# Performance work log

Hardware: AMD Instinct MI355X
Metric: run time of the kernel (lower is better)

## Reference

```python
import jax, jax.numpy as jnp
import numpy as np

SCALING = 128.0 / 64  # alpha / rank = 2.0
EPS = 1e-8


def setup_inputs() -> dict:
    key = jax.random.key(0)
    ks = jax.random.split(key, 5)
    B, S, D_IN, D_OUT, R = 2, 4096, 4096, 4096, 64
    x = jax.random.normal(ks[0], (B, S, D_IN), dtype=jnp.float32)
    base_output = jax.random.normal(ks[1], (B, S, D_OUT), dtype=jnp.float32)
    base_weight = jax.random.normal(ks[2], (D_OUT, D_IN), dtype=jnp.float32) * 0.02
    lora_A = jax.random.normal(ks[3], (R, D_IN), dtype=jnp.float32) * 0.02
    lora_B = jax.random.normal(ks[4], (D_OUT, R), dtype=jnp.float32) * 0.02
    magnitude = jnp.ones((D_OUT,), dtype=jnp.float32)
    return {"x": x, "base_output": base_output, "base_weight": base_weight,
            "lora_A": lora_A, "lora_B": lora_B, "magnitude": magnitude}


def reference(x, base_output, base_weight, lora_A, lora_B, magnitude):
    # LoRA path: x @ A^T @ B^T, scaled  (dropout p=0 -> identity)
    xa = jnp.einsum('bsd,rd->bsr', x, lora_A)          # [B,S,r]
    delta_v = jnp.einsum('bsr,or->bso', xa, lora_B) * SCALING  # [B,S,out]
    # Updated weight and its per-row L2 norm
    updated_weight = base_weight + (lora_B @ lora_A) * SCALING  # [out,in]
    updated_norm = jnp.sqrt(jnp.sum(updated_weight * updated_weight, axis=1))  # [out]
    mag_scale = magnitude / (updated_norm + EPS)  # [out]
    combined = base_output + delta_v
    return combined * mag_scale[None, None, :]
```

## Files before the change

### kernel.cpp

```cpp
#include <hip/hip_runtime.h>
#include <math.h>

typedef __bf16 bf16x8 __attribute__((ext_vector_type(8)));
typedef float f32x4 __attribute__((ext_vector_type(4)));

#define MFMA16(a, b, c) __builtin_amdgcn_mfma_f32_16x16x32_bf16(a, b, c, 0, 0, 0)

static constexpr int M_TOT = 8192;
static constexpr int DIN = 4096;
static constexpr int DOUT = 4096;
static constexpr int RNK = 64;

__device__ inline unsigned short f2bf(float f) {
    union { float f; unsigned u; } v; v.f = f;
    unsigned r = v.u + 0x7FFFu + ((v.u >> 16) & 1u);
    return (unsigned short)(r >> 16);
}

__device__ inline void gload_lds16(const float* g, char* lds_base) {
    __builtin_amdgcn_global_load_lds(
        (const __attribute__((address_space(1))) void*)g,
        (__attribute__((address_space(3))) void*)lds_base, 16, 0, 0);
}

__global__ __launch_bounds__(256) void k_prep(const float* __restrict__ A,
                                              const float* __restrict__ B,
                                              unsigned short* __restrict__ Afrag,
                                              unsigned short* __restrict__ Atfrag,
                                              unsigned short* __restrict__ Bfrag) {
    int i = blockIdx.x * 256 + threadIdx.x;
    unsigned short ab = f2bf(A[i]);
    int n = i >> 12, k = i & 4095;
    Afrag[(((k >> 5) << 2) + (n >> 4)) * 512 +
          ((((k >> 3) & 3) << 4) + (n & 15)) * 8 + (k & 7)] = ab;
    Atfrag[(((k >> 4) << 1) + (n >> 5)) * 512 +
           ((((n >> 3) & 3) << 4) + (k & 15)) * 8 + (n & 7)] = ab;
    unsigned short bb = f2bf(B[i]);
    int o = i >> 6, r = i & 63;
    Bfrag[(((o >> 4) << 1) + (r >> 5)) * 512 +
          ((((r >> 3) & 3) << 4) + (o & 15)) * 8 + (r & 7)] = bb;
}

__global__ __launch_bounds__(256) void k1_xa(const float* __restrict__ x,
                                             const unsigned short* __restrict__ Afrag,
                                             float* __restrict__ pxa) {
    __shared__ __align__(16) char smem[32768];
    char* buf0 = smem;
    char* buf1 = smem + 16384;
    float (*red)[1024] = (float (*)[1024])smem;
    int tid = threadIdx.x;
    int wid = tid >> 6, lane = tid & 63;
    int row = lane & 15, kq = lane >> 4;
    int lane8 = lane * 8;
    int mt = blockIdx.x & 511, kpart = blockIdx.x >> 9;
    int m0 = mt * 16;
    int swzr = (row & 7) << 4;
    const float* xbase = x + (size_t)m0 * DIN + kpart * 2048;

    f32x4 acc0 = {0.f, 0.f, 0.f, 0.f};
    f32x4 acc1 = acc0, acc2 = acc0, acc3 = acc0;
    bf16x8 setA[8], setB[8];

    auto STAGE = [&](char* buf, int c) {
        #pragma unroll
        for (int j = 0; j < 4; ++j) {
            int r = wid * 4 + j;
            int srcb = (lane * 16) ^ ((r & 7) << 4);
            const float* g = xbase + (size_t)r * DIN + c * 256 + (srcb >> 2);
            gload_lds16(g, buf + r * 1024);
        }
    };
    auto AFRAG = [&](bf16x8* set, int c) {
        #pragma unroll
        for (int s = 0; s < 2; ++s) {
            int ks = kpart * 64 + c * 8 + wid * 2 + s;
            const unsigned short* ap = Afrag + (size_t)ks * 2048 + lane8;
            set[s * 4 + 0] = *(const bf16x8*)(ap);
            set[s * 4 + 1] = *(const bf16x8*)(ap + 512);
            set[s * 4 + 2] = *(const bf16x8*)(ap + 1024);
            set[s * 4 + 3] = *(const bf16x8*)(ap + 1536);
        }
    };
    auto COMPUTE = [&](const char* buf, const bf16x8* set) {
        #pragma unroll
        for (int s = 0; s < 2; ++s) {
            int kbyte = wid * 256 + s * 128 + kq * 32;
            f32x4 xlo = *(const f32x4*)(buf + row * 1024 + ((kbyte) ^ swzr));
            f32x4 xhi = *(const f32x4*)(buf + row * 1024 + ((kbyte + 16) ^ swzr));
            bf16x8 af;
            #pragma unroll
            for (int j = 0; j < 4; ++j) {
                af[j] = (__bf16)xlo[j];
                af[j + 4] = (__bf16)xhi[j];
            }
            acc0 = MFMA16(af, set[s * 4 + 0], acc0);
            acc1 = MFMA16(af, set[s * 4 + 1], acc1);
            acc2 = MFMA16(af, set[s * 4 + 2], acc2);
            acc3 = MFMA16(af, set[s * 4 + 3], acc3);
        }
    };

    STAGE(buf0, 0); AFRAG(setA, 0);
    __syncthreads();
    #pragma unroll
    for (int c = 0; c < 8; c += 2) {
        if (c + 1 < 8) { STAGE(buf1, c + 1); AFRAG(setB, c + 1); }
        COMPUTE(buf0, setA);
        __syncthreads();
        if (c + 2 < 8) { STAGE(buf0, c + 2); AFRAG(setA, c + 2); }
        if (c + 1 < 8) COMPUTE(buf1, setB);
        __syncthreads();
    }

    int mb = kq * 4;
    #pragma unroll
    for (int rg = 0; rg < 4; ++rg) {
        red[wid][(mb + rg) * 64 + row]      = acc0[rg];
        red[wid][(mb + rg) * 64 + 16 + row] = acc1[rg];
        red[wid][(mb + rg) * 64 + 32 + row] = acc2[rg];
        red[wid][(mb + rg) * 64 + 48 + row] = acc3[rg];
    }
    __syncthreads();
    #pragma unroll
    for (int e = tid; e < 1024; e += 256) {
        float s = red[0][e] + red[1][e] + red[2][e] + red[3][e];
        pxa[(size_t)kpart * M_TOT * RNK + (size_t)(m0 + (e >> 6)) * RNK + (e & 63)] = s;
    }
}

__global__ __launch_bounds__(256) void k1_fin(const float* __restrict__ pxa,
                                              unsigned short* __restrict__ xafrag) {
    int tid = threadIdx.x;
    int mt = blockIdx.x;
    int e0 = tid * 4;
    size_t o = (size_t)(mt * 16 + (e0 >> 6)) * RNK + (e0 & 63);
    f32x4 s0 = *(const f32x4*)(pxa + o);
    f32x4 s1 = *(const f32x4*)(pxa + (size_t)M_TOT * RNK + o);
    int ml = e0 >> 6, r0 = e0 & 63;
    ushort4 h;
    h.x = f2bf(s0[0] + s1[0]);
    h.y = f2bf(s0[1] + s1[1]);
    h.z = f2bf(s0[2] + s1[2]);
    h.w = f2bf(s0[3] + s1[3]);
    *(ushort4*)&xafrag[((size_t)(mt * 2 + (r0 >> 5))) * 512 +
                       ((((r0 >> 3) & 3) << 4) + ml) * 8 + (r0 & 7)] = h;
}

__global__ __launch_bounds__(256) void k2_norm(const float* __restrict__ bw,
                                               const unsigned short* __restrict__ Bfrag,
                                               const unsigned short* __restrict__ Atfrag,
                                               float* __restrict__ pn) {
    __shared__ __align__(16) char smem[32768];
    __shared__ float part[4][16];
    char* buf0 = smem;
    char* buf1 = smem + 16384;
    int tid = threadIdx.x;
    int wid = tid >> 6, lane = tid & 63;
    int row = lane & 15, kq = lane >> 4;
    int lane8 = lane * 8;
    int ot = blockIdx.x & 255, ipart = blockIdx.x >> 8;
    int o0 = ot * 16;
    int swzr = (row & 7) << 4;
    const float* bwbase = bw + (size_t)o0 * DIN + ipart * 1024;

    bf16x8 b0 = *(const bf16x8*)(Bfrag + (size_t)(ot * 2) * 512 + lane8);
    bf16x8 b1 = *(const bf16x8*)(Bfrag + (size_t)(ot * 2 + 1) * 512 + lane8);

    f32x4 nacc = {0.f, 0.f, 0.f, 0.f};
    bf16x8 setA[8], setB[8];

    auto STAGE = [&](char* buf, int c) {
        #pragma unroll
        for (int j = 0; j < 4; ++j) {
            int r = wid * 4 + j;
            int srcb = (lane * 16) ^ ((r & 7) << 4);
            const float* g = bwbase + (size_t)r * DIN + c * 256 + (srcb >> 2);
            gload_lds16(g, buf + r * 1024);
        }
    };
    auto ATFRAG = [&](bf16x8* set, int c) {
        #pragma unroll
        for (int g = 0; g < 4; ++g) {
            int it = ipart * 64 + c * 16 + wid * 4 + g;
            const unsigned short* atp = Atfrag + (size_t)it * 1024 + lane8;
            set[g * 2]     = *(const bf16x8*)(atp);
            set[g * 2 + 1] = *(const bf16x8*)(atp + 512);
        }
    };
    auto COMPUTE = [&](const char* buf, const bf16x8* set) {
        #pragma unroll
        for (int g = 0; g < 4; ++g) {
            f32x4 d = {0.f, 0.f, 0.f, 0.f};
            d = MFMA16(set[g * 2], b0, d);
            d = MFMA16(set[g * 2 + 1], b1, d);
            int ibyte = wid * 256 + g * 64 + kq * 16;
            f32x4 wv = *(const f32x4*)(buf + row * 1024 + (ibyte ^ swzr));
            #pragma unroll
            for (int rg = 0; rg < 4; ++rg) {
                float w = wv[rg] + 2.0f * d[rg];
                nacc[rg] += w * w;
            }
        }
    };

    STAGE(buf0, 0); ATFRAG(setA, 0);
    __syncthreads();
    #pragma unroll
    for (int c = 0; c < 4; c += 2) {
        if (c + 1 < 4) { STAGE(buf1, c + 1); ATFRAG(setB, c + 1); }
        COMPUTE(buf0, setA);
        __syncthreads();
        if (c + 2 < 4) { STAGE(buf0, c + 2); ATFRAG(setA, c + 2); }
        if (c + 1 < 4) COMPUTE(buf1, setB);
        __syncthreads();
    }

    float ns = nacc[0] + nacc[1] + nacc[2] + nacc[3];
    ns += __shfl_xor(ns, 16, 64);
    ns += __shfl_xor(ns, 32, 64);
    if (kq == 0) part[wid][row] = ns;
    __syncthreads();
    if (tid < 16)
        pn[ipart * DOUT + o0 + tid] =
            part[0][tid] + part[1][tid] + part[2][tid] + part[3][tid];
}

__global__ __launch_bounds__(256) void k2b_scale(const float* __restrict__ pn,
                                                 const float* __restrict__ mag,
                                                 float* __restrict__ mscale) {
    int o = blockIdx.x * 256 + threadIdx.x;
    float n2 = 0.f;
    #pragma unroll
    for (int p = 0; p < 4; ++p) n2 += pn[p * DOUT + o];
    mscale[o] = mag[o] / (sqrtf(n2) + 1e-8f);
}

__global__ __launch_bounds__(256) void kB(const float* __restrict__ base,
                                          const unsigned short* __restrict__ xafrag,
                                          const unsigned short* __restrict__ Bfrag,
                                          const float* __restrict__ mscale,
                                          float* __restrict__ out) {
    __shared__ float dls[32][260];
    int tid = threadIdx.x;
    int wid = tid >> 6, lane = tid & 63;
    int row = lane & 15, kq = lane >> 4;
    int m0 = blockIdx.x * 32;
    int n0 = blockIdx.y * 256;
    int col = n0 + lane * 4;
    int lane8 = lane * 8;

    f32x4 bpre[2][4];
    #pragma unroll
    for (int h = 0; h < 2; ++h)
        #pragma unroll
        for (int r = 0; r < 4; ++r)
            bpre[h][r] = __builtin_nontemporal_load(
                (const f32x4*)(base + (size_t)(m0 + h * 16 + wid * 4 + r) * DOUT + col));
    f32x4 msv = *(const f32x4*)(mscale + col);

    bf16x8 xb0[2], xb1[2];
    #pragma unroll
    for (int h = 0; h < 2; ++h) {
        size_t mt = (size_t)(blockIdx.x * 2 + h);
        xb0[h] = *(const bf16x8*)(xafrag + (mt * 2) * 512 + lane8);
        xb1[h] = *(const bf16x8*)(xafrag + (mt * 2 + 1) * 512 + lane8);
    }

    #pragma unroll
    for (int nt = 0; nt < 4; ++nt) {
        size_t ntg = (size_t)((n0 + wid * 64 + nt * 16) >> 4);
        bf16x8 a0 = *(const bf16x8*)(Bfrag + (ntg * 2) * 512 + lane8);
        bf16x8 a1 = *(const bf16x8*)(Bfrag + (ntg * 2 + 1) * 512 + lane8);
        #pragma unroll
        for (int h = 0; h < 2; ++h) {
            f32x4 acc = {0.f, 0.f, 0.f, 0.f};
            acc = MFMA16(a0, xb0[h], acc);
            acc = MFMA16(a1, xb1[h], acc);
            *(f32x4*)&dls[h * 16 + row][wid * 64 + nt * 16 + kq * 4] = acc;
        }
    }
    __syncthreads();

    #pragma unroll
    for (int h = 0; h < 2; ++h)
        #pragma unroll
        for (int r = 0; r < 4; ++r) {
            int m = h * 16 + wid * 4 + r;
            f32x4 d = *(const f32x4*)&dls[m][lane * 4];
            size_t gidx = (size_t)(m0 + m) * DOUT + col;
            f32x4 o;
            #pragma unroll
            for (int j = 0; j < 4; ++j) o[j] = (bpre[h][r][j] + 2.0f * d[j]) * msv[j];
            __builtin_nontemporal_store(o, (f32x4*)(out + gidx));
        }
}

extern "C" void kernel_launch(void* const* d_in, const int* in_sizes, int n_in,
                              void* d_out, int out_size, void* d_ws, size_t ws_size,
                              hipStream_t stream) {
    const float* x    = (const float*)d_in[0];
    const float* base = (const float*)d_in[1];
    const float* bw   = (const float*)d_in[2];
    const float* lA   = (const float*)d_in[3];
    const float* lB   = (const float*)d_in[4];
    const float* mag  = (const float*)d_in[5];
    float* out = (float*)d_out;

    char* ws = (char*)d_ws;
    unsigned short* Afrag  = (unsigned short*)(ws);
    unsigned short* Atfrag = (unsigned short*)(ws + (512u << 10));
    unsigned short* Bfrag  = (unsigned short*)(ws + (1024u << 10));
    unsigned short* xafrag = (unsigned short*)(ws + (1536u << 10));
    float*          pxa    = (float*)(ws + (2560u << 10));
    float*          pn     = (float*)(ws + (6656u << 10));
    float*          msc    = (float*)(ws + (6720u << 10));

    hipLaunchKernelGGL(k_prep, dim3(1024), dim3(256), 0, stream, lA, lB, Afrag, Atfrag, Bfrag);
    hipLaunchKernelGGL(k1_xa, dim3(1024), dim3(256), 0, stream, x, Afrag, pxa);
    hipLaunchKernelGGL(k2_norm, dim3(1024), dim3(256), 0, stream, bw, Bfrag, Atfrag, pn);
    hipLaunchKernelGGL(k1_fin, dim3(512), dim3(256), 0, stream, pxa, xafrag);
    hipLaunchKernelGGL(k2b_scale, dim3(DOUT / 256), dim3(256), 0, stream, pn, mag, msc);
    hipLaunchKernelGGL(kB, dim3(M_TOT / 32, DOUT / 256), dim3(256), 0, stream,
                       base, xafrag, Bfrag, msc, out);
}
```

Measured before the change: 113.4 us.

## Merge xA projection and weight-norm kernels into one heterogeneous launch

Fuses the x·Aᵀ partial-product kernel and the updated-weight row-norm kernel into a single launch. The first 256 blocks each compute a full norm over the input dimension, with no ipart split, and the remaining 1024 blocks do the xA work. The two finishing kernels are likewise merged into one launch. This cuts four launches to two and lets the bandwidth-heavy norm and xA work run concurrently. The cost is that each norm block now does four times longer serial work, which could leave a long tail in the merged grid.

New measurement: 109.9 us. -3.1%, faster.

```diff
diff --git a/kernel.cpp b/kernel.cpp
--- a/kernel.cpp
+++ b/kernel.cpp
@@ -41,198 +41,191 @@
           ((((r >> 3) & 3) << 4) + (o & 15)) * 8 + (r & 7)] = bb;
 }
 
-__global__ __launch_bounds__(256) void k1_xa(const float* __restrict__ x,
-                                             const unsigned short* __restrict__ Afrag,
-                                             float* __restrict__ pxa) {
-    __shared__ __align__(16) char smem[32768];
-    char* buf0 = smem;
-    char* buf1 = smem + 16384;
-    float (*red)[1024] = (float (*)[1024])smem;
-    int tid = threadIdx.x;
-    int wid = tid >> 6, lane = tid & 63;
-    int row = lane & 15, kq = lane >> 4;
-    int lane8 = lane * 8;
-    int mt = blockIdx.x & 511, kpart = blockIdx.x >> 9;
-    int m0 = mt * 16;
-    int swzr = (row & 7) << 4;
-    const float* xbase = x + (size_t)m0 * DIN + kpart * 2048;
-
-    f32x4 acc0 = {0.f, 0.f, 0.f, 0.f};
-    f32x4 acc1 = acc0, acc2 = acc0, acc3 = acc0;
-    bf16x8 setA[8], setB[8];
-
-    auto STAGE = [&](char* buf, int c) {
-        #pragma unroll
-        for (int j = 0; j < 4; ++j) {
-            int r = wid * 4 + j;
-            int srcb = (lane * 16) ^ ((r & 7) << 4);
-            const float* g = xbase + (size_t)r * DIN + c * 256 + (srcb >> 2);
-            gload_lds16(g, buf + r * 1024);
-        }
-    };
-    auto AFRAG = [&](bf16x8* set, int c) {
-        #pragma unroll
-        for (int s = 0; s < 2; ++s) {
-            int ks = kpart * 64 + c * 8 + wid * 2 + s;
-            const unsigned short* ap = Afrag + (size_t)ks * 2048 + lane8;
-            set[s * 4 + 0] = *(const bf16x8*)(ap);
-            set[s * 4 + 1] = *(const bf16x8*)(ap + 512);
-            set[s * 4 + 2] = *(const bf16x8*)(ap + 1024);
-            set[s * 4 + 3] = *(const bf16x8*)(ap + 1536);
-        }
-    };
-    auto COMPUTE = [&](const char* buf, const bf16x8* set) {
-        #pragma unroll
-        for (int s = 0; s < 2; ++s) {
-            int kbyte = wid * 256 + s * 128 + kq * 32;
-            f32x4 xlo = *(const f32x4*)(buf + row * 1024 + ((kbyte) ^ swzr));
-            f32x4 xhi = *(const f32x4*)(buf + row * 1024 + ((kbyte + 16) ^ swzr));
-            bf16x8 af;
-            #pragma unroll
-            for (int j = 0; j < 4; ++j) {
-                af[j] = (__bf16)xlo[j];
-                af[j + 4] = (__bf16)xhi[j];
-            }
-            acc0 = MFMA16(af, set[s * 4 + 0], acc0);
-            acc1 = MFMA16(af, set[s * 4 + 1], acc1);
-            acc2 = MFMA16(af, set[s * 4 + 2], acc2);
-            acc3 = MFMA16(af, set[s * 4 + 3], acc3);
-        }
-    };
-
-    STAGE(buf0, 0); AFRAG(setA, 0);
-    __syncthreads();
-    #pragma unroll
-    for (int c = 0; c < 8; c += 2) {
-        if (c + 1 < 8) { STAGE(buf1, c + 1); AFRAG(setB, c + 1); }
-        COMPUTE(buf0, setA);
-        __syncthreads();
-        if (c + 2 < 8) { STAGE(buf0, c + 2); AFRAG(setA, c + 2); }
-        if (c + 1 < 8) COMPUTE(buf1, setB);
-        __syncthreads();
-    }
-
-    int mb = kq * 4;
-    #pragma unroll
-    for (int rg = 0; rg < 4; ++rg) {
-        red[wid][(mb + rg) * 64 + row]      = acc0[rg];
-        red[wid][(mb + rg) * 64 + 16 + row] = acc1[rg];
-        red[wid][(mb + rg) * 64 + 32 + row] = acc2[rg];
-        red[wid][(mb + rg) * 64 + 48 + row] = acc3[rg];
-    }
-    __syncthreads();
-    #pragma unroll
-    for (int e = tid; e < 1024; e += 256) {
-        float s = red[0][e] + red[1][e] + red[2][e] + red[3][e];
-        pxa[(size_t)kpart * M_TOT * RNK + (size_t)(m0 + (e >> 6)) * RNK + (e & 63)] = s;
-    }
-}
-
-__global__ __launch_bounds__(256) void k1_fin(const float* __restrict__ pxa,
-                                              unsigned short* __restrict__ xafrag) {
-    int tid = threadIdx.x;
-    int mt = blockIdx.x;
-    int e0 = tid * 4;
-    size_t o = (size_t)(mt * 16 + (e0 >> 6)) * RNK + (e0 & 63);
-    f32x4 s0 = *(const f32x4*)(pxa + o);
-    f32x4 s1 = *(const f32x4*)(pxa + (size_t)M_TOT * RNK + o);
-    int ml = e0 >> 6, r0 = e0 & 63;
-    ushort4 h;
-    h.x = f2bf(s0[0] + s1[0]);
-    h.y = f2bf(s0[1] + s1[1]);
-    h.z = f2bf(s0[2] + s1[2]);
-    h.w = f2bf(s0[3] + s1[3]);
-    *(ushort4*)&xafrag[((size_t)(mt * 2 + (r0 >> 5))) * 512 +
-                       ((((r0 >> 3) & 3) << 4) + ml) * 8 + (r0 & 7)] = h;
-}
-
-__global__ __launch_bounds__(256) void k2_norm(const float* __restrict__ bw,
-                                               const unsigned short* __restrict__ Bfrag,
-                                               const unsigned short* __restrict__ Atfrag,
-                                               float* __restrict__ pn) {
-    __shared__ __align__(16) char smem[32768];
-    __shared__ float part[4][16];
+__global__ __launch_bounds__(256) void kAB(const float* __restrict__ x,
+                                           const unsigned short* __restrict__ Afrag,
+                                           float* __restrict__ pxa,
+                                           const float* __restrict__ bw,
+                                           const unsigned short* __restrict__ Bfrag,
+                                           const unsigned short* __restrict__ Atfrag,
+                                           float* __restrict__ pn) {
+    __shared__ __align__(16) char smem[33024];
     char* buf0 = smem;
     char* buf1 = smem + 16384;
     int tid = threadIdx.x;
     int wid = tid >> 6, lane = tid & 63;
     int row = lane & 15, kq = lane >> 4;
     int lane8 = lane * 8;
-    int ot = blockIdx.x & 255, ipart = blockIdx.x >> 8;
-    int o0 = ot * 16;
     int swzr = (row & 7) << 4;
-    const float* bwbase = bw + (size_t)o0 * DIN + ipart * 1024;
-
-    bf16x8 b0 = *(const bf16x8*)(Bfrag + (size_t)(ot * 2) * 512 + lane8);
-    bf16x8 b1 = *(const bf16x8*)(Bfrag + (size_t)(ot * 2 + 1) * 512 + lane8);
-
-    f32x4 nacc = {0.f, 0.f, 0.f, 0.f};
-    bf16x8 setA[8], setB[8];
-
-    auto STAGE = [&](char* buf, int c) {
-        #pragma unroll
-        for (int j = 0; j < 4; ++j) {
-            int r = wid * 4 + j;
-            int srcb = (lane * 16) ^ ((r & 7) << 4);
-            const float* g = bwbase + (size_t)r * DIN + c * 256 + (srcb >> 2);
-            gload_lds16(g, buf + r * 1024);
-        }
-    };
-    auto ATFRAG = [&](bf16x8* set, int c) {
-        #pragma unroll
-        for (int g = 0; g < 4; ++g) {
-            int it = ipart * 64 + c * 16 + wid * 4 + g;
-            const unsigned short* atp = Atfrag + (size_t)it * 1024 + lane8;
-            set[g * 2]     = *(const bf16x8*)(atp);
-            set[g * 2 + 1] = *(const bf16x8*)(atp + 512);
-        }
-    };
-    auto COMPUTE = [&](const char* buf, const bf16x8* set) {
-        #pragma unroll
-        for (int g = 0; g < 4; ++g) {
-            f32x4 d = {0.f, 0.f, 0.f, 0.f};
-            d = MFMA16(set[g * 2], b0, d);
-            d = MFMA16(set[g * 2 + 1], b1, d);
-            int ibyte = wid * 256 + g * 64 + kq * 16;
-            f32x4 wv = *(const f32x4*)(buf + row * 1024 + (ibyte ^ swzr));
-            #pragma unroll
-            for (int rg = 0; rg < 4; ++rg) {
-                float w = wv[rg] + 2.0f * d[rg];
-                nacc[rg] += w * w;
-            }
-        }
-    };
-
-    STAGE(buf0, 0); ATFRAG(setA, 0);
-    __syncthreads();
-    #pragma unroll
-    for (int c = 0; c < 4; c += 2) {
-        if (c + 1 < 4) { STAGE(buf1, c + 1); ATFRAG(setB, c + 1); }
-        COMPUTE(buf0, setA);
+
+    if (blockIdx.x >= 256) {
+        int bid = blockIdx.x - 256;
+        float (*red)[1024] = (float (*)[1024])smem;
+        int mt = bid & 511, kpart = bid >> 9;
+        int m0 = mt * 16;
+        const float* xbase = x + (size_t)m0 * DIN + kpart * 2048;
+
+        f32x4 acc0 = {0.f, 0.f, 0.f, 0.f};
+        f32x4 acc1 = acc0, acc2 = acc0, acc3 = acc0;
+        bf16x8 setA[8], setB[8];
+
+        auto STAGE = [&](char* buf, int c) {
+            #pragma unroll
+            for (int j = 0; j < 4; ++j) {
+                int r = wid * 4 + j;
+                int srcb = (lane * 16) ^ ((r & 7) << 4);
+                const float* g = xbase + (size_t)r * DIN + c * 256 + (srcb >> 2);
+                gload_lds16(g, buf + r * 1024);
+            }
+        };
+        auto AFRAG = [&](bf16x8* set, int c) {
+            #pragma unroll
+            for (int s = 0; s < 2; ++s) {
+                int ks = kpart * 64 + c * 8 + wid * 2 + s;
+                const unsigned short* ap = Afrag + (size_t)ks * 2048 + lane8;
+                set[s * 4 + 0] = *(const bf16x8*)(ap);
+                set[s * 4 + 1] = *(const bf16x8*)(ap + 512);
+                set[s * 4 + 2] = *(const bf16x8*)(ap + 1024);
+                set[s * 4 + 3] = *(const bf16x8*)(ap + 1536);
+            }
+        };
+        auto COMPUTE = [&](const char* buf, const bf16x8* set) {
+            #pragma unroll
+            for (int s = 0; s < 2; ++s) {
+                int kbyte = wid * 256 + s * 128 + kq * 32;
+                f32x4 xlo = *(const f32x4*)(buf + row * 1024 + ((kbyte) ^ swzr));
+                f32x4 xhi = *(const f32x4*)(buf + row * 1024 + ((kbyte + 16) ^ swzr));
+                bf16x8 af;
+                #pragma unroll
+                for (int j = 0; j < 4; ++j) {
+                    af[j] = (__bf16)xlo[j];
+                    af[j + 4] = (__bf16)xhi[j];
+                }
+                acc0 = MFMA16(af, set[s * 4 + 0], acc0);
+                acc1 = MFMA16(af, set[s * 4 + 1], acc1);
+                acc2 = MFMA16(af, set[s * 4 + 2], acc2);
+                acc3 = MFMA16(af, set[s * 4 + 3], acc3);
+            }
+        };
+
+        STAGE(buf0, 0); AFRAG(setA, 0);
         __syncthreads();
-        if (c + 2 < 4) { STAGE(buf0, c + 2); ATFRAG(setA, c + 2); }
-        if (c + 1 < 4) COMPUTE(buf1, setB);
+        #pragma unroll
+        for (int c = 0; c < 8; c += 2) {
+            if (c + 1 < 8) { STAGE(buf1, c + 1); AFRAG(setB, c + 1); }
+            COMPUTE(buf0, setA);
+            __syncthreads();
+            if (c + 2 < 8) { STAGE(buf0, c + 2); AFRAG(setA, c + 2); }
+            if (c + 1 < 8) COMPUTE(buf1, setB);
+            __syncthreads();
+        }
+
+        int mb = kq * 4;
+        #pragma unroll
+        for (int rg = 0; rg < 4; ++rg) {
+            red[wid][(mb + rg) * 64 + row]      = acc0[rg];
+            red[wid][(mb + rg) * 64 + 16 + row] = acc1[rg];
+            red[wid][(mb + rg) * 64 + 32 + row] = acc2[rg];
+            red[wid][(mb + rg) * 64 + 48 + row] = acc3[rg];
+        }
         __syncthreads();
+        #pragma unroll
+        for (int e = tid; e < 1024; e += 256) {
+            float s = red[0][e] + red[1][e] + red[2][e] + red[3][e];
+            pxa[(size_t)kpart * M_TOT * RNK + (size_t)(m0 + (e >> 6)) * RNK + (e & 63)] = s;
+        }
+    } else {
+        int bid = blockIdx.x;
+        float (*part)[16] = (float (*)[16])(smem + 32768);
+        int ot = bid & 255, ipart = 0;
+        int o0 = ot * 16;
+        const float* bwbase = bw + (size_t)o0 * DIN;
+
+        bf16x8 b0 = *(const bf16x8*)(Bfrag + (size_t)(ot * 2) * 512 + lane8);
+        bf16x8 b1 = *(const bf16x8*)(Bfrag + (size_t)(ot * 2 + 1) * 512 + lane8);
+
+        f32x4 nacc = {0.f, 0.f, 0.f, 0.f};
+        bf16x8 setA[8], setB[8];
+
+        auto STAGE = [&](char* buf, int c) {
+            #pragma unroll
+            for (int j = 0; j < 4; ++j) {
+                int r = wid * 4 + j;
+                int srcb = (lane * 16) ^ ((r & 7) << 4);
+                const float* g = bwbase + (size_t)r * DIN + c * 256 + (srcb >> 2);
+                gload_lds16(g, buf + r * 1024);
+            }
+        };
+        auto ATFRAG = [&](bf16x8* set, int c) {
+            #pragma unroll
+            for (int g = 0; g < 4; ++g) {
+                int it = c * 16 + wid * 4 + g;
+                const unsigned short* atp = Atfrag + (size_t)it * 1024 + lane8;
+                set[g * 2]     = *(const bf16x8*)(atp);
+                set[g * 2 + 1] = *(const bf16x8*)(atp + 512);
+            }
+        };
+        auto COMPUTE = [&](const char* buf, const bf16x8* set) {
+            #pragma unroll
+            for (int g = 0; g < 4; ++g) {
+                f32x4 d = {0.f, 0.f, 0.f, 0.f};
+                d = MFMA16(set[g * 2], b0, d);
+                d = MFMA16(set[g * 2 + 1], b1, d);
+                int ibyte = wid * 256 + g * 64 + kq * 16;
+                f32x4 wv = *(const f32x4*)(buf + row * 1024 + (ibyte ^ swzr));
+                #pragma unroll
+                for (int rg = 0; rg < 4; ++rg) {
+                    float w = wv[rg] + 2.0f * d[rg];
+                    nacc[rg] += w * w;
+                }
+            }
+        };
+
+        STAGE(buf0, 0); ATFRAG(setA, 0);
+        __syncthreads();
+        #pragma unroll 2
+        for (int c = 0; c < 16; c += 2) {
+            if (c + 1 < 16) { STAGE(buf1, c + 1); ATFRAG(setB, c + 1); }
+            COMPUTE(buf0, setA);
+            __syncthreads();
+            if (c + 2 < 16) { STAGE(buf0, c + 2); ATFRAG(setA, c + 2); }
+            if (c + 1 < 16) COMPUTE(buf1, setB);
+            __syncthreads();
+        }
+
+        float ns = nacc[0] + nacc[1] + nacc[2] + nacc[3];
+        ns += __shfl_xor(ns, 16, 64);
+        ns += __shfl_xor(ns, 32, 64);
+        if (kq == 0) part[wid][row] = ns;
+        __syncthreads();
+        if (tid < 16)
+            pn[o0 + tid] = part[0][tid] + part[1][tid] + part[2][tid] + part[3][tid];
     }
-
-    float ns = nacc[0] + nacc[1] + nacc[2] + nacc[3];
-    ns += __shfl_xor(ns, 16, 64);
-    ns += __shfl_xor(ns, 32, 64);
-    if (kq == 0) part[wid][row] = ns;
-    __syncthreads();
-    if (tid < 16)
-        pn[ipart * DOUT + o0 + tid] =
-            part[0][tid] + part[1][tid] + part[2][tid] + part[3][tid];
-}
-
-__global__ __launch_bounds__(256) void k2b_scale(const float* __restrict__ pn,
-                                                 const float* __restrict__ mag,
-                                                 float* __restrict__ mscale) {
-    int o = blockIdx.x * 256 + threadIdx.x;
-    float n2 = 0.f;
-    #pragma unroll
-    for (int p = 0; p < 4; ++p) n2 += pn[p * DOUT + o];
-    mscale[o] = mag[o] / (sqrtf(n2) + 1e-8f);
+}
+
+__global__ __launch_bounds__(256) void kfin(const float* __restrict__ pxa,
+                                            unsigned short* __restrict__ xafrag,
+                                            const float* __restrict__ pn,
+                                            const float* __restrict__ mag,
+                                            float* __restrict__ mscale) {
+    int tid = threadIdx.x;
+    if (blockIdx.x < 512) {
+        int mt = blockIdx.x;
+        int e0 = tid * 4;
+        size_t o = (size_t)(mt * 16 + (e0 >> 6)) * RNK + (e0 & 63);
+        f32x4 s0 = *(const f32x4*)(pxa + o);
+        f32x4 s1 = *(const f32x4*)(pxa + (size_t)M_TOT * RNK + o);
+        int ml = e0 >> 6, r0 = e0 & 63;
+        ushort4 h;
+        h.x = f2bf(s0[0] + s1[0]);
+        h.y = f2bf(s0[1] + s1[1]);
+        h.z = f2bf(s0[2] + s1[2]);
+        h.w = f2bf(s0[3] + s1[3]);
+        *(ushort4*)&xafrag[((size_t)(mt * 2 + (r0 >> 5))) * 512 +
+                           ((((r0 >> 3) & 3) << 4) + ml) * 8 + (r0 & 7)] = h;
+    } else {
+        int o = (int)(blockIdx.x - 512) * 256 + tid;
+        mscale[o] = mag[o] / (sqrtf(pn[o]) + 1e-8f);
+    }
 }
 
 __global__ __launch_bounds__(256) void kB(const float* __restrict__ base,
@@ -316,10 +309,9 @@
     float*          msc    = (float*)(ws + (6720u << 10));
 
     hipLaunchKernelGGL(k_prep, dim3(1024), dim3(256), 0, stream, lA, lB, Afrag, Atfrag, Bfrag);
-    hipLaunchKernelGGL(k1_xa, dim3(1024), dim3(256), 0, stream, x, Afrag, pxa);
-    hipLaunchKernelGGL(k2_norm, dim3(1024), dim3(256), 0, stream, bw, Bfrag, Atfrag, pn);
-    hipLaunchKernelGGL(k1_fin, dim3(512), dim3(256), 0, stream, pxa, xafrag);
-    hipLaunchKernelGGL(k2b_scale, dim3(DOUT / 256), dim3(256), 0, stream, pn, mag, msc);
+    hipLaunchKernelGGL(kAB, dim3(1280), dim3(256), 0, stream,
+                       x, Afrag, pxa, bw, Bfrag, Atfrag, pn);
+    hipLaunchKernelGGL(kfin, dim3(528), dim3(256), 0, stream, pxa, xafrag, pn, mag, msc);
     hipLaunchKernelGGL(kB, dim3(M_TOT / 32, DOUT / 256), dim3(256), 0, stream,
                        base, xafrag, Bfrag, msc, out);
 }
```
